# Optimization experiments

Measured on AMD Instinct MI355X. Metric: run time of the kernel, lower is better.

Reference implementation:

```python
import jax, jax.numpy as jnp
import numpy as np

B, N, F_IN = 8, 4096, 32
NRP = 1024
D_MODEL = 512
K = 64  # max_num_neighbors
STAGE_CFG = ((1024, 0.05), (256, 0.3), (64, 0.5))  # (num_samples=ceil(0.25*N_in), radius)


def fps(pos, m):
    """Farthest point sampling of m points from pos (N,3), deterministic start at 0."""
    d = jnp.sum((pos - pos[0]) ** 2, axis=-1)
    idxs = jnp.zeros((m,), jnp.int32)
    def body(i, carry):
        idxs, d = carry
        nxt = jnp.argmax(d).astype(jnp.int32)
        d = jnp.minimum(d, jnp.sum((pos - pos[nxt]) ** 2, axis=-1))
        return (idxs.at[i].set(nxt), d)
    idxs, _ = jax.lax.fori_loop(1, m, body, (idxs, d))
    return idxs


def apply_mlp(h, ws, bs):
    for w, b in zip(ws[:-1], bs[:-1]):
        h = jax.nn.relu(h @ w + b)
    return h @ ws[-1] + bs[-1]


def sa_stage(x, pos, m, r, ws, bs):
    """SAModule: FPS -> radius neighbors (<=K) -> PointNetConv (gather, MLP, max-scatter)."""
    idx = jax.vmap(lambda p: fps(p, m))(pos)                          # (B,m)
    pos_s = jnp.take_along_axis(pos, idx[..., None], axis=1)          # (B,m,3)
    d2 = jnp.sum((pos_s[:, :, None, :] - pos[:, None, :, :]) ** 2, -1)  # (B,m,N)
    neg = jnp.where(d2 <= r * r, -d2, -jnp.inf)
    vals, nbr = jax.lax.top_k(neg, K)                                 # (B,m,K) nearest within r
    valid = vals > -jnp.inf                                           # self always valid (d2=0)
    x_j = jax.vmap(lambda xb, nb: xb[nb])(x, nbr)                     # (B,m,K,F) gather
    p_j = jax.vmap(lambda pb, nb: pb[nb])(pos, nbr)                   # (B,m,K,3)
    h = jnp.concatenate([x_j, p_j - pos_s[:, :, None, :]], axis=-1)   # message input
    h = apply_mlp(h, ws, bs)
    h = jnp.where(valid[..., None], h, -jnp.inf)
    return jnp.max(h, axis=2), pos_s                                  # max aggregation


def _forward(point_cloud_features, point_cloud, emb_table, point_id_emb, stage_params):
    x = emb_table[point_cloud_features[..., 0]]                       # (B,N,F_IN)
    x = x.at[:, :NRP].add(point_id_emb)
    pos = point_cloud
    for (m, r), (ws, bs) in zip(STAGE_CFG, stage_params):
        x, pos = sa_stage(x, pos, m, r, ws, bs)
    return x, pos                                                     # (B,64,D_MODEL), (B,64,3)


def setup_inputs() -> dict:
    key = jax.random.key(0)
    ks = iter(jax.random.split(key, 64))
    def nrm(shape, s=0.05):
        return s * jax.random.normal(next(ks), shape, dtype=jnp.float32)
    inp = {
        "point_cloud_features": jax.random.randint(next(ks), (B, N, 1), 0, 3),
        "point_cloud": jax.random.uniform(next(ks), (B, N, 3), dtype=jnp.float32),
        "emb_table": nrm((3, F_IN), 1.0),
        "point_id_emb": nrm((1, NRP, F_IN), 1.0),
    }
    dims = {"s1": [3 + F_IN, 64, 64, 64], "s2": [64 + 3, 128, 128, 256], "s3": [256 + 3, 256, 512, D_MODEL]}
    for s, d in dims.items():
        for i in range(3):
            inp[f"{s}w{i}"] = nrm((d[i], d[i + 1]))
            inp[f"{s}b{i}"] = jnp.zeros((d[i + 1],), jnp.float32)
    return inp


def reference(point_cloud_features, point_cloud, emb_table, point_id_emb,
              s1w0, s1b0, s1w1, s1b1, s1w2, s1b2,
              s2w0, s2b0, s2w1, s2b1, s2w2, s2b2,
              s3w0, s3b0, s3w1, s3b1, s3w2, s3b2):
    stage_params = [
        ([s1w0, s1w1, s1w2], [s1b0, s1b1, s1b2]),
        ([s2w0, s2w1, s2w2], [s2b0, s2b1, s2b2]),
        ([s3w0, s3w1, s3w2], [s3b0, s3b1, s3b2]),
    ]
    return _forward(point_cloud_features, point_cloud, emb_table, point_id_emb, stage_params)
```

## Files before the change

kernel.cpp:

```cpp
#include <hip/hip_runtime.h>

#define DEVI static __device__ __forceinline__

constexpr int B = 8;
constexpr int N0 = 4096;
constexpr int KNB = 64;

typedef float f32x2 __attribute__((ext_vector_type(2)));

DEVI float dist2f(float ax, float ay, float az, float bx, float by, float bz) {
#pragma clang fp contract(off)
  float dx = ax - bx;
  float dy = ay - by;
  float dz = az - bz;
  return (dx * dx + dy * dy) + dz * dz;
}
DEVI f32x2 dist2v(f32x2 ax, f32x2 ay, f32x2 az, float bx, float by, float bz) {
#pragma clang fp contract(off)
  f32x2 dx = ax - bx;
  f32x2 dy = ay - by;
  f32x2 dz = az - bz;
  return (dx * dx + dy * dy) + dz * dz;
}

DEVI unsigned long long packMinKey(float v, int i) {
  return ((unsigned long long)__float_as_uint(v) << 32) | (unsigned int)i;
}

template <int CTRL, int RM>
DEVI float dppMaxF32(float v) {
  int o = __builtin_amdgcn_update_dpp(__float_as_int(v), __float_as_int(v),
                                      CTRL, RM, 0xf, false);
  return fmaxf(v, __int_as_float(o));
}
DEVI float waveMaxF32(float v) {
  v = dppMaxF32<0x111, 0xf>(v);
  v = dppMaxF32<0x112, 0xf>(v);
  v = dppMaxF32<0x114, 0xf>(v);
  v = dppMaxF32<0x118, 0xf>(v);
  v = dppMaxF32<0x142, 0xa>(v);
  v = dppMaxF32<0x143, 0xc>(v);
  return __int_as_float(__builtin_amdgcn_readlane(__float_as_int(v), 63));
}
template <int CTRL, int RM>
DEVI unsigned dppMinU32(unsigned v) {
  int o = __builtin_amdgcn_update_dpp((int)v, (int)v, CTRL, RM, 0xf, false);
  unsigned ov = (unsigned)o;
  return v < ov ? v : ov;
}
DEVI unsigned waveMinU32(unsigned v) {
  v = dppMinU32<0x111, 0xf>(v);
  v = dppMinU32<0x112, 0xf>(v);
  v = dppMinU32<0x114, 0xf>(v);
  v = dppMinU32<0x118, 0xf>(v);
  v = dppMinU32<0x142, 0xa>(v);
  v = dppMinU32<0x143, 0xc>(v);
  return (unsigned)__builtin_amdgcn_readlane((int)v, 63);
}


DEVI void x0_body(const int* __restrict__ feat, const float* __restrict__ emb,
                  const float* __restrict__ pid, float* __restrict__ x0buf,
                  int bx, int t) {
  int gid = bx * 256 + t;
  if (gid >= B * N0 * 32) return;
  int c = gid & 31;
  int bn = gid >> 5;
  int n = bn & (N0 - 1);
  int f = feat[bn];
  float v = emb[f * 32 + c];
  if (n < 1024) v += pid[n * 32 + c];
  x0buf[gid] = v;
}

template <int NPTS, int M, int BLK>
DEVI void fps_body(char* smem, const float* __restrict__ pos,
                   float* __restrict__ pos_out, int b, int t) {
  constexpr int EPT = NPTS / BLK;
  constexpr int EP2 = EPT / 2;
  constexpr int NW = BLK / 64;
  float4* posl = (float4*)smem;
  float4* outp = (float4*)(smem + (size_t)NPTS * 16);
  unsigned long long* redk =
      (unsigned long long*)(smem + (size_t)(NPTS + M) * 16);
  const float* pb = pos + (size_t)b * NPTS * 3;
  f32x2 px[EP2], py[EP2], pz[EP2], d[EP2];
#pragma unroll
  for (int e = 0; e < EP2; ++e) {
    int i0 = t + (2 * e) * BLK;
    int i1 = t + (2 * e + 1) * BLK;
    float x0 = pb[i0 * 3 + 0], y0 = pb[i0 * 3 + 1], z0 = pb[i0 * 3 + 2];
    float x1 = pb[i1 * 3 + 0], y1 = pb[i1 * 3 + 1], z1 = pb[i1 * 3 + 2];
    px[e] = (f32x2){x0, x1};
    py[e] = (f32x2){y0, y1};
    pz[e] = (f32x2){z0, z1};
    posl[i0] = make_float4(x0, y0, z0, 0.f);
    posl[i1] = make_float4(x1, y1, z1, 0.f);
  }
  float sx = pb[0], sy = pb[1], sz = pb[2];
  if (t == 0) outp[0] = make_float4(sx, sy, sz, 0.f);
  f32x2 m2 = (f32x2){-1.f, -1.f};
#pragma unroll
  for (int e = 0; e < EP2; ++e) {
    d[e] = dist2v(px[e], py[e], pz[e], sx, sy, sz);
    m2.x = fmaxf(m2.x, d[e].x);
    m2.y = fmaxf(m2.y, d[e].y);
  }
  for (int it = 1; it < M; ++it) {
    const float vstar = waveMaxF32(fmaxf(m2.x, m2.y));
    unsigned cand = 0xffffffffu;
#pragma unroll
    for (int e = 0; e < EP2; ++e) {
      unsigned c0 = (d[e].x == vstar) ? (unsigned)(t + (2 * e) * BLK) : 0xffffffffu;
      unsigned c1 = (d[e].y == vstar) ? (unsigned)(t + (2 * e + 1) * BLK) : 0xffffffffu;
      cand = cand < c0 ? cand : c0;
      cand = cand < c1 ? cand : c1;
    }
    cand = waveMinU32(cand);
    unsigned sel;
    if constexpr (NW > 1) {
      if ((t & 63) == 0) {
        unsigned long long key =
            ((unsigned long long)__float_as_uint(vstar) << 32) |
            (unsigned)(0x7fffffffu - cand);
        redk[(it & 1) * NW + (t >> 6)] = key;
      }
      __syncthreads();
      unsigned long long kk = redk[(it & 1) * NW + 0];
#pragma unroll
      for (int w = 1; w < NW; ++w) {
        unsigned long long o = redk[(it & 1) * NW + w];
        kk = (kk > o) ? kk : o;
      }
      sel = 0x7fffffffu - (unsigned)(kk & 0xffffffffULL);
    } else {
      sel = cand;
    }
    float4 sp = posl[sel];
    if (t == 0) outp[it] = sp;
    m2 = (f32x2){-1.f, -1.f};
#pragma unroll
    for (int e = 0; e < EP2; ++e) {
      f32x2 nd = dist2v(px[e], py[e], pz[e], sp.x, sp.y, sp.z);
      d[e].x = fminf(d[e].x, nd.x);
      d[e].y = fminf(d[e].y, nd.y);
      m2.x = fmaxf(m2.x, d[e].x);
      m2.y = fmaxf(m2.y, d[e].y);
    }
  }
  if constexpr (NW > 1) __syncthreads();
  for (int m = t; m < M; m += BLK) {
    float4 q = outp[m];
    pos_out[(size_t)(b * M + m) * 3 + 0] = q.x;
    pos_out[(size_t)(b * M + m) * 3 + 1] = q.y;
    pos_out[(size_t)(b * M + m) * 3 + 2] = q.z;
  }
}

template <int NPTS, int M>
DEVI void radius_body(char* smem, const float* __restrict__ pos,
                      const float* __restrict__ pos_s, float r2,
                      int* __restrict__ nbr, int* __restrict__ cnt, int blk,
                      int t) {
  unsigned long long* candkey = (unsigned long long*)smem;
  int* ctrp = (int*)(smem + (size_t)NPTS * 8);
  const int b = blk / M;
  const float* pb = pos + (size_t)b * NPTS * 3;
  const float cx = pos_s[(size_t)blk * 3 + 0];
  const float cy = pos_s[(size_t)blk * 3 + 1];
  const float cz = pos_s[(size_t)blk * 3 + 2];
  if (t == 0) *ctrp = 0;
  __syncthreads();
  for (int j = t; j < NPTS; j += 256) {
    float d2 = dist2f(pb[j * 3 + 0], pb[j * 3 + 1], pb[j * 3 + 2], cx, cy, cz);
    if (d2 <= r2) {
      int p = atomicAdd(ctrp, 1);
      candkey[p] = packMinKey(d2, j);
      if (p < KNB) nbr[(size_t)blk * KNB + p] = j;
    }
  }
  __syncthreads();
  const int c = *ctrp;
  if (c <= KNB) {
    if (t == 0) cnt[blk] = c;
    return;
  }
  for (int s = t; s < c; s += 256) {
    unsigned long long mykey = candkey[s];
    int rank = 0;
#pragma unroll 4
    for (int j = 0; j < c; ++j) {
      rank += (candkey[j] < mykey) ? 1 : 0;
    }
    if (rank < KNB)
      nbr[(size_t)blk * KNB + rank] = (int)(unsigned)(mykey & 0xffffffffULL);
  }
  if (t == 0) cnt[blk] = KNB;
}

DEVI void conv1_body(char* smem, const float* __restrict__ x0buf,
                     const float* __restrict__ pos,
                     const float* __restrict__ pos_s,
                     const int* __restrict__ nbr, const int* __restrict__ cntp,
                     const float* __restrict__ w0, const float* __restrict__ b0,
                     const float* __restrict__ w1, const float* __restrict__ b1,
                     const float* __restrict__ w2, const float* __restrict__ b2,
                     float* __restrict__ x1, int blk, int t) {
  float(*ins)[36] = (float(*)[36])smem;
  float(*hh)[65] = (float(*)[65])(smem + 576);
  float(*sred)[65] = (float(*)[65])(smem + 1616);
  const int slot = t >> 6;
  const int ch = t & 63;
  const int b = blk >> 10;
  const int c = cntp[blk];
  const float cx = pos_s[(size_t)blk * 3 + 0];
  const float cy = pos_s[(size_t)blk * 3 + 1];
  const float cz = pos_s[(size_t)blk * 3 + 2];
  float best = -__builtin_inff();
  for (int r0 = 0; r0 < c; r0 += 4) {
    const int r = r0 + slot;
    const bool act = r < c;
    const int j = nbr[(size_t)blk * KNB + (act ? r : 0)];
    if (ch < 32) {
      ins[slot][ch] = x0buf[((size_t)(b * N0) + j) * 32 + ch];
    } else if (ch < 35) {
      float pv = pos[((size_t)(b * N0) + j) * 3 + (ch - 32)];
      float cv = (ch == 32) ? cx : (ch == 33) ? cy : cz;
      ins[slot][ch] = pv - cv;
    }
    __syncthreads();
    float v = b0[ch];
#pragma unroll
    for (int i = 0; i < 35; ++i) v = fmaf(ins[slot][i], w0[i * 64 + ch], v);
    v = fmaxf(v, 0.f);
    hh[slot][ch] = v;
    __syncthreads();
    float v2 = b1[ch];
#pragma unroll
    for (int i = 0; i < 64; ++i) v2 = fmaf(hh[slot][i], w1[i * 64 + ch], v2);
    v2 = fmaxf(v2, 0.f);
    __syncthreads();
    hh[slot][ch] = v2;
    __syncthreads();
    float v3 = b2[ch];
#pragma unroll
    for (int i = 0; i < 64; ++i) v3 = fmaf(hh[slot][i], w2[i * 64 + ch], v3);
    if (act) best = fmaxf(best, v3);
    __syncthreads();
  }
  sred[slot][ch] = best;
  __syncthreads();
  if (t < 64) {
    float v = sred[0][t];
#pragma unroll
    for (int s = 1; s < 4; ++s) v = fmaxf(v, sred[s][t]);
    x1[(size_t)blk * 64 + t] = v;
  }
}

DEVI void conv2_body(char* smem, const float* __restrict__ x1,
                     const float* __restrict__ pos1,
                     const float* __restrict__ pos2,
                     const int* __restrict__ nbr, const int* __restrict__ cntp,
                     const float* __restrict__ w0, const float* __restrict__ b0,
                     const float* __restrict__ w1, const float* __restrict__ b1,
                     const float* __restrict__ w2, const float* __restrict__ b2,
                     float* __restrict__ x2, int blk, int t) {
  float(*msg)[68] = (float(*)[68])smem;
  float(*h)[128] = (float(*)[128])(smem + 17408);
  float(*red)[256] = (float(*)[256])(smem + 17408 + 32768);
  const int b = blk >> 8;
  const int c = cntp[blk];
  const float cx = pos2[(size_t)blk * 3 + 0];
  const float cy = pos2[(size_t)blk * 3 + 1];
  const float cz = pos2[(size_t)blk * 3 + 2];
  for (int idx = t; idx < 64 * 68; idx += 256) {
    int r = idx / 68;
    int k = idx - r * 68;
    float v = 0.f;
    if (r < c && k < 67) {
      int j = nbr[(size_t)blk * KNB + r];
      if (k < 64) {
        v = x1[((size_t)(b * 1024) + j) * 64 + k];
      } else {
        float pv = pos1[((size_t)(b * 1024) + j) * 3 + (k - 64)];
        v = pv - ((k == 64) ? cx : (k == 65) ? cy : cz);
      }
    }
    msg[r][k] = v;
  }
  __syncthreads();
  const int rg = t >> 5;
  const int cg = t & 31;
  {
    float acc[8][4] = {};
    for (int i4 = 0; i4 < 16; ++i4) {
      float wv[4][4];
#pragma unroll
      for (int k = 0; k < 4; ++k) {
        float4 q = *(const float4*)&w0[(size_t)(i4 * 4 + k) * 128 + cg * 4];
        wv[k][0] = q.x; wv[k][1] = q.y; wv[k][2] = q.z; wv[k][3] = q.w;
      }
#pragma unroll
      for (int rr = 0; rr < 8; ++rr) {
        float4 aq = *(const float4*)&msg[rg * 8 + rr][i4 * 4];
        float a[4] = {aq.x, aq.y, aq.z, aq.w};
#pragma unroll
        for (int k = 0; k < 4; ++k)
#pragma unroll
          for (int cc = 0; cc < 4; ++cc)
            acc[rr][cc] = fmaf(a[k], wv[k][cc], acc[rr][cc]);
      }
    }
#pragma unroll
    for (int i = 64; i < 67; ++i) {
      float wv[4];
#pragma unroll
      for (int cc = 0; cc < 4; ++cc) wv[cc] = w0[(size_t)i * 128 + cg * 4 + cc];
#pragma unroll
      for (int rr = 0; rr < 8; ++rr) {
        float a = msg[rg * 8 + rr][i];
#pragma unroll
        for (int cc = 0; cc < 4; ++cc) acc[rr][cc] = fmaf(a, wv[cc], acc[rr][cc]);
      }
    }
#pragma unroll
    for (int rr = 0; rr < 8; ++rr)
#pragma unroll
      for (int cc = 0; cc < 4; ++cc)
        h[rg * 8 + rr][cg * 4 + cc] = fmaxf(acc[rr][cc] + b0[cg * 4 + cc], 0.f);
  }
  __syncthreads();
  {
    float acc[8][4] = {};
    for (int i4 = 0; i4 < 32; ++i4) {
      float wv[4][4];
#pragma unroll
      for (int k = 0; k < 4; ++k) {
        float4 q = *(const float4*)&w1[(size_t)(i4 * 4 + k) * 128 + cg * 4];
        wv[k][0] = q.x; wv[k][1] = q.y; wv[k][2] = q.z; wv[k][3] = q.w;
      }
#pragma unroll
      for (int rr = 0; rr < 8; ++rr) {
        float4 aq = *(const float4*)&h[rg * 8 + rr][i4 * 4];
        float a[4] = {aq.x, aq.y, aq.z, aq.w};
#pragma unroll
        for (int k = 0; k < 4; ++k)
#pragma unroll
          for (int cc = 0; cc < 4; ++cc)
            acc[rr][cc] = fmaf(a[k], wv[k][cc], acc[rr][cc]);
      }
    }
    __syncthreads();
#pragma unroll
    for (int rr = 0; rr < 8; ++rr)
#pragma unroll
      for (int cc = 0; cc < 4; ++cc)
        h[rg * 8 + rr][cg * 4 + cc] = fmaxf(acc[rr][cc] + b1[cg * 4 + cc], 0.f);
  }
  __syncthreads();
  {
    float acc[8][8] = {};
    for (int i4 = 0; i4 < 32; ++i4) {
      float wv[4][8];
#pragma unroll
      for (int k = 0; k < 4; ++k) {
        float4 q0 = *(const float4*)&w2[(size_t)(i4 * 4 + k) * 256 + cg * 8];
        float4 q1 = *(const float4*)&w2[(size_t)(i4 * 4 + k) * 256 + cg * 8 + 4];
        wv[k][0] = q0.x; wv[k][1] = q0.y; wv[k][2] = q0.z; wv[k][3] = q0.w;
        wv[k][4] = q1.x; wv[k][5] = q1.y; wv[k][6] = q1.z; wv[k][7] = q1.w;
      }
#pragma unroll
      for (int rr = 0; rr < 8; ++rr) {
        float4 aq = *(const float4*)&h[rg * 8 + rr][i4 * 4];
        float a[4] = {aq.x, aq.y, aq.z, aq.w};
#pragma unroll
        for (int k = 0; k < 4; ++k)
#pragma unroll
          for (int cc = 0; cc < 8; ++cc)
            acc[rr][cc] = fmaf(a[k], wv[k][cc], acc[rr][cc]);
      }
    }
    float mx[8];
#pragma unroll
    for (int cc = 0; cc < 8; ++cc) mx[cc] = -__builtin_inff();
#pragma unroll
    for (int rr = 0; rr < 8; ++rr) {
      if (rg * 8 + rr < c) {
#pragma unroll
        for (int cc = 0; cc < 8; ++cc)
          mx[cc] = fmaxf(mx[cc], acc[rr][cc] + b2[cg * 8 + cc]);
      }
    }
#pragma unroll
    for (int cc = 0; cc < 8; ++cc) red[rg][cg * 8 + cc] = mx[cc];
  }
  __syncthreads();
  {
    float v = red[0][t];
#pragma unroll
    for (int g = 1; g < 8; ++g) v = fmaxf(v, red[g][t]);
    x2[(size_t)blk * 256 + t] = v;
  }
}


__global__ void __launch_bounds__(256) l1_kernel(
    const float* __restrict__ pos, float* __restrict__ pos1,
    const int* __restrict__ feat, const float* __restrict__ emb,
    const float* __restrict__ pid, float* __restrict__ x0buf) {
  __shared__ __attribute__((aligned(16))) char smem[81984];
  if (blockIdx.x < 8) {
    fps_body<4096, 1024, 256>(smem, pos, pos1, blockIdx.x, threadIdx.x);
  } else {
    x0_body(feat, emb, pid, x0buf, blockIdx.x - 8, threadIdx.x);
  }
}

__global__ void __launch_bounds__(256) l2_kernel(
    const float* __restrict__ pos1, float* __restrict__ pos2,
    const float* __restrict__ pos, float r2a, int* __restrict__ nbr1,
    int* __restrict__ cnt1) {
  __shared__ __attribute__((aligned(16))) char smem[33024];
  if (blockIdx.x < 8) {
    fps_body<1024, 256, 256>(smem, pos1, pos2, blockIdx.x, threadIdx.x);
  } else {
    radius_body<4096, 1024>(smem, pos, pos1, r2a, nbr1, cnt1, blockIdx.x - 8,
                            threadIdx.x);
  }
}

__global__ void __launch_bounds__(256) l3_kernel(
    const float* __restrict__ pos2, float* __restrict__ pos3, float r2b,
    int* __restrict__ nbr2, int* __restrict__ cnt2,
    const float* __restrict__ pos1, const float* __restrict__ x0buf,
    const float* __restrict__ pos, const int* __restrict__ nbr1,
    const int* __restrict__ cnt1, const float* __restrict__ w0,
    const float* __restrict__ b0, const float* __restrict__ w1,
    const float* __restrict__ b1, const float* __restrict__ w2,
    const float* __restrict__ b2, float* __restrict__ x1) {
  __shared__ __attribute__((aligned(16))) char smem[8448];
  if (blockIdx.x < 8) {
    if (threadIdx.x < 64)
      fps_body<256, 64, 64>(smem, pos2, pos3, blockIdx.x, threadIdx.x);
  } else if (blockIdx.x < 8 + 2048) {
    radius_body<1024, 256>(smem, pos1, pos2, r2b, nbr2, cnt2, blockIdx.x - 8,
                           threadIdx.x);
  } else {
    conv1_body(smem, x0buf, pos, pos1, nbr1, cnt1, w0, b0, w1, b1, w2, b2, x1,
               blockIdx.x - (8 + 2048), threadIdx.x);
  }
}

__global__ void __launch_bounds__(256) l4_kernel(
    const float* __restrict__ pos2, const float* __restrict__ pos3, float r2c,
    int* __restrict__ nbr3, int* __restrict__ cnt3,
    const float* __restrict__ x1, const float* __restrict__ pos1,
    const int* __restrict__ nbr2, const int* __restrict__ cnt2,
    const float* __restrict__ w0, const float* __restrict__ b0,
    const float* __restrict__ w1, const float* __restrict__ b1,
    const float* __restrict__ w2, const float* __restrict__ b2,
    float* __restrict__ x2) {
  __shared__ __attribute__((aligned(16))) char smem[58368];
  if (blockIdx.x < 512) {
    radius_body<256, 64>(smem, pos2, pos3, r2c, nbr3, cnt3, blockIdx.x,
                         threadIdx.x);
  } else {
    conv2_body(smem, x1, pos1, pos2, nbr2, cnt2, w0, b0, w1, b1, w2, b2, x2,
               blockIdx.x - 512, threadIdx.x);
  }
}

__global__ void __launch_bounds__(256) conv3_kernel(
    const float* __restrict__ x2, const float* __restrict__ pos2,
    const float* __restrict__ pos3, const int* __restrict__ nbr,
    const int* __restrict__ cntp,
    const float* __restrict__ w0, const float* __restrict__ b0,
    const float* __restrict__ w1, const float* __restrict__ b1,
    const float* __restrict__ w2, const float* __restrict__ b2,
    float* __restrict__ out) {
  __shared__ __attribute__((aligned(16))) float msg[16][260];
  __shared__ __attribute__((aligned(16))) float h[16][512];
  __shared__ float red[4][512];
  __shared__ float omax[512];
  const int blk = blockIdx.x;
  const int t = threadIdx.x;
  const int b = blk >> 6;
  const int c = cntp[blk];
  const float cx = pos3[(size_t)blk * 3 + 0];
  const float cy = pos3[(size_t)blk * 3 + 1];
  const float cz = pos3[(size_t)blk * 3 + 2];
  omax[t] = -__builtin_inff();
  omax[t + 256] = -__builtin_inff();
  const int rg = t >> 6;
  const int cg = t & 63;
  __syncthreads();
  for (int ch = 0; ch < 4; ++ch) {
    if (ch * 16 >= c) break;
    for (int idx = t; idx < 16 * 260; idx += 256) {
      int r = idx / 260;
      int k = idx - r * 260;
      int rglob = ch * 16 + r;
      float v = 0.f;
      if (rglob < c && k < 259) {
        int j = nbr[(size_t)blk * KNB + rglob];
        if (k < 256) {
          v = x2[((size_t)(b * 256) + j) * 256 + k];
        } else {
          float pv = pos2[((size_t)(b * 256) + j) * 3 + (k - 256)];
          v = pv - ((k == 256) ? cx : (k == 257) ? cy : cz);
        }
      }
      msg[r][k] = v;
    }
    __syncthreads();
    {
      float acc[4][4] = {};
      for (int i4 = 0; i4 < 64; ++i4) {
        float wv[4][4];
#pragma unroll
        for (int k = 0; k < 4; ++k) {
          float4 q = *(const float4*)&w0[(size_t)(i4 * 4 + k) * 256 + cg * 4];
          wv[k][0] = q.x; wv[k][1] = q.y; wv[k][2] = q.z; wv[k][3] = q.w;
        }
#pragma unroll
        for (int rr = 0; rr < 4; ++rr) {
          float4 aq = *(const float4*)&msg[rg * 4 + rr][i4 * 4];
          float a[4] = {aq.x, aq.y, aq.z, aq.w};
#pragma unroll
          for (int k = 0; k < 4; ++k)
#pragma unroll
            for (int cc = 0; cc < 4; ++cc)
              acc[rr][cc] = fmaf(a[k], wv[k][cc], acc[rr][cc]);
        }
      }
#pragma unroll
      for (int i = 256; i < 259; ++i) {
        float wv[4];
#pragma unroll
        for (int cc = 0; cc < 4; ++cc) wv[cc] = w0[(size_t)i * 256 + cg * 4 + cc];
#pragma unroll
        for (int rr = 0; rr < 4; ++rr) {
          float a = msg[rg * 4 + rr][i];
#pragma unroll
          for (int cc = 0; cc < 4; ++cc) acc[rr][cc] = fmaf(a, wv[cc], acc[rr][cc]);
        }
      }
#pragma unroll
      for (int rr = 0; rr < 4; ++rr)
#pragma unroll
        for (int cc = 0; cc < 4; ++cc)
          h[rg * 4 + rr][cg * 4 + cc] = fmaxf(acc[rr][cc] + b0[cg * 4 + cc], 0.f);
    }
    __syncthreads();
    {
      float acc[4][8] = {};
      for (int i4 = 0; i4 < 64; ++i4) {
        float wv[4][8];
#pragma unroll
        for (int k = 0; k < 4; ++k) {
          float4 q0 = *(const float4*)&w1[(size_t)(i4 * 4 + k) * 512 + cg * 8];
          float4 q1 = *(const float4*)&w1[(size_t)(i4 * 4 + k) * 512 + cg * 8 + 4];
          wv[k][0] = q0.x; wv[k][1] = q0.y; wv[k][2] = q0.z; wv[k][3] = q0.w;
          wv[k][4] = q1.x; wv[k][5] = q1.y; wv[k][6] = q1.z; wv[k][7] = q1.w;
        }
#pragma unroll
        for (int rr = 0; rr < 4; ++rr) {
          float4 aq = *(const float4*)&h[rg * 4 + rr][i4 * 4];
          float a[4] = {aq.x, aq.y, aq.z, aq.w};
#pragma unroll
          for (int k = 0; k < 4; ++k)
#pragma unroll
            for (int cc = 0; cc < 8; ++cc)
              acc[rr][cc] = fmaf(a[k], wv[k][cc], acc[rr][cc]);
        }
      }
      __syncthreads();
#pragma unroll
      for (int rr = 0; rr < 4; ++rr)
#pragma unroll
        for (int cc = 0; cc < 8; ++cc)
          h[rg * 4 + rr][cg * 8 + cc] = fmaxf(acc[rr][cc] + b1[cg * 8 + cc], 0.f);
    }
    __syncthreads();
    {
      float acc[4][8] = {};
      for (int i4 = 0; i4 < 128; ++i4) {
        float wv[4][8];
#pragma unroll
        for (int k = 0; k < 4; ++k) {
          float4 q0 = *(const float4*)&w2[(size_t)(i4 * 4 + k) * 512 + cg * 8];
          float4 q1 = *(const float4*)&w2[(size_t)(i4 * 4 + k) * 512 + cg * 8 + 4];
          wv[k][0] = q0.x; wv[k][1] = q0.y; wv[k][2] = q0.z; wv[k][3] = q0.w;
          wv[k][4] = q1.x; wv[k][5] = q1.y; wv[k][6] = q1.z; wv[k][7] = q1.w;
        }
#pragma unroll
        for (int rr = 0; rr < 4; ++rr) {
          float4 aq = *(const float4*)&h[rg * 4 + rr][i4 * 4];
          float a[4] = {aq.x, aq.y, aq.z, aq.w};
#pragma unroll
          for (int k = 0; k < 4; ++k)
#pragma unroll
            for (int cc = 0; cc < 8; ++cc)
              acc[rr][cc] = fmaf(a[k], wv[k][cc], acc[rr][cc]);
        }
      }
      float mx[8];
#pragma unroll
      for (int cc = 0; cc < 8; ++cc) mx[cc] = -__builtin_inff();
#pragma unroll
      for (int rr = 0; rr < 4; ++rr) {
        if (ch * 16 + rg * 4 + rr < c) {
#pragma unroll
          for (int cc = 0; cc < 8; ++cc)
            mx[cc] = fmaxf(mx[cc], acc[rr][cc] + b2[cg * 8 + cc]);
        }
      }
#pragma unroll
      for (int cc = 0; cc < 8; ++cc) red[rg][cg * 8 + cc] = mx[cc];
    }
    __syncthreads();
    for (int k = t; k < 512; k += 256) {
      float v = omax[k];
#pragma unroll
      for (int g = 0; g < 4; ++g) v = fmaxf(v, red[g][k]);
      omax[k] = v;
    }
    __syncthreads();
  }
  out[(size_t)blk * 512 + t] = omax[t];
  out[(size_t)blk * 512 + t + 256] = omax[t + 256];
}

extern "C" void kernel_launch(void* const* d_in, const int* in_sizes, int n_in,
                              void* d_out, int out_size, void* d_ws, size_t ws_size,
                              hipStream_t stream) {
  const int* feat = (const int*)d_in[0];
  const float* pos = (const float*)d_in[1];
  const float* emb = (const float*)d_in[2];
  const float* pid = (const float*)d_in[3];
  const float* s1w0 = (const float*)d_in[4];
  const float* s1b0 = (const float*)d_in[5];
  const float* s1w1 = (const float*)d_in[6];
  const float* s1b1 = (const float*)d_in[7];
  const float* s1w2 = (const float*)d_in[8];
  const float* s1b2 = (const float*)d_in[9];
  const float* s2w0 = (const float*)d_in[10];
  const float* s2b0 = (const float*)d_in[11];
  const float* s2w1 = (const float*)d_in[12];
  const float* s2b1 = (const float*)d_in[13];
  const float* s2w2 = (const float*)d_in[14];
  const float* s2b2 = (const float*)d_in[15];
  const float* s3w0 = (const float*)d_in[16];
  const float* s3b0 = (const float*)d_in[17];
  const float* s3w1 = (const float*)d_in[18];
  const float* s3b1 = (const float*)d_in[19];
  const float* s3w2 = (const float*)d_in[20];
  const float* s3b2 = (const float*)d_in[21];
  (void)in_sizes; (void)n_in; (void)out_size; (void)ws_size;

  char* ws = (char*)d_ws;
  size_t off = 0;
  auto alloc = [&](size_t nbytes) {
    void* p = ws + off;
    off = (off + nbytes + 255) & ~(size_t)255;
    return p;
  };
  float* x0 = (float*)alloc((size_t)B * N0 * 32 * 4);
  float* pos1 = (float*)alloc((size_t)B * 1024 * 3 * 4);
  int* nbr1 = (int*)alloc((size_t)B * 1024 * KNB * 4);
  int* cnt1 = (int*)alloc((size_t)B * 1024 * 4);
  float* x1 = (float*)alloc((size_t)B * 1024 * 64 * 4);
  float* pos2 = (float*)alloc((size_t)B * 256 * 3 * 4);
  int* nbr2 = (int*)alloc((size_t)B * 256 * KNB * 4);
  int* cnt2 = (int*)alloc((size_t)B * 256 * 4);
  float* x2 = (float*)alloc((size_t)B * 256 * 256 * 4);
  int* nbr3 = (int*)alloc((size_t)B * 64 * KNB * 4);
  int* cnt3 = (int*)alloc((size_t)B * 64 * 4);

  float* xout = (float*)d_out;
  float* pos3 = xout + (size_t)B * 64 * 512;

  const float r2a = (float)(0.05 * 0.05);
  const float r2b = (float)(0.3 * 0.3);
  const float r2c = (float)(0.5 * 0.5);

  l1_kernel<<<8 + 4096, 256, 0, stream>>>(pos, pos1, feat, emb, pid, x0);
  l2_kernel<<<8 + 8192, 256, 0, stream>>>(pos1, pos2, pos, r2a, nbr1, cnt1);
  l3_kernel<<<8 + 2048 + 8192, 256, 0, stream>>>(
      pos2, pos3, r2b, nbr2, cnt2, pos1, x0, pos, nbr1, cnt1,
      s1w0, s1b0, s1w1, s1b1, s1w2, s1b2, x1);
  l4_kernel<<<512 + 2048, 256, 0, stream>>>(
      pos2, pos3, r2c, nbr3, cnt3, x1, pos1, nbr2, cnt2,
      s2w0, s2b0, s2w1, s2b1, s2w2, s2b2, x2);
  conv3_kernel<<<B * 64, 256, 0, stream>>>(x2, pos2, pos3, nbr3, cnt3,
                                           s3w0, s3b0, s3w1, s3b1, s3w2, s3b2, xout);
}
```

Measured before the change: 1.517 ms.

## Run stage-3 PointNet MLP on bf16 MFMA with split hi/lo precision

Replaces the scalar-FMA conv3 kernel with one that uses 16x16x32 bf16 MFMA instructions. Each fp32 operand is split into bf16 hi and lo parts, and three MFMAs per tile keep accuracy close to fp32. Per-call pack kernels pre-swizzle the stage-3 weights into fragment layout. The kernel processes all 64 neighbors at once, tiles layer 2 and layer 3 by output chunk, and uses a cross-wave max reduction. It adds three small kernel launches and some precision risk from the bf16x3 emulation.

After: 1.460 ms. -3.7%, faster.

```diff
diff --git a/kernel.cpp b/kernel.cpp
--- a/kernel.cpp
+++ b/kernel.cpp
@@ -7,6 +7,8 @@
 constexpr int KNB = 64;
 
 typedef float f32x2 __attribute__((ext_vector_type(2)));
+typedef float f32x4 __attribute__((ext_vector_type(4)));
+typedef short bf16x8 __attribute__((ext_vector_type(8)));
 
 DEVI float dist2f(float ax, float ay, float az, float bx, float by, float bz) {
 #pragma clang fp contract(off)
@@ -56,6 +58,23 @@
   v = dppMinU32<0x142, 0xa>(v);
   v = dppMinU32<0x143, 0xc>(v);
   return (unsigned)__builtin_amdgcn_readlane((int)v, 63);
+}
+
+DEVI unsigned short bfhi(float x) {
+  unsigned u = __float_as_uint(x);
+  return (unsigned short)((u + 0x7FFFu + ((u >> 16) & 1u)) >> 16);
+}
+DEVI float bf2f(unsigned short h) { return __uint_as_float(((unsigned)h) << 16); }
+DEVI void mkfrag(const float* p, bf16x8& hi, bf16x8& lo) {
+#pragma unroll
+  for (int e = 0; e < 8; ++e) {
+    float x = p[e];
+    unsigned short h = bfhi(x);
+    float r = x - bf2f(h);
+    unsigned short l2 = bfhi(r);
+    hi[e] = (short)h;
+    lo[e] = (short)l2;
+  }
 }
 
 
@@ -471,165 +490,170 @@
   }
 }
 
-__global__ void __launch_bounds__(256) conv3_kernel(
+__global__ void __launch_bounds__(256) pack_kernel(
+    const float* __restrict__ W, int Kreal, int KS, int N,
+    unsigned short* __restrict__ hi, unsigned short* __restrict__ lo) {
+  int gid = blockIdx.x * 256 + threadIdx.x;
+  int total = (N / 16) * KS * 64 * 8;
+  if (gid >= total) return;
+  int e = gid & 7;
+  int l = (gid >> 3) & 63;
+  int rest = gid >> 9;
+  int ks = rest % KS;
+  int nt = rest / KS;
+  int n = nt * 16 + (l & 15);
+  int k = ks * 32 + (l >> 4) * 8 + e;
+  float val = (k < Kreal) ? W[(size_t)k * N + n] : 0.f;
+  unsigned short h = bfhi(val);
+  float r = val - bf2f(h);
+  hi[gid] = h;
+  lo[gid] = bfhi(r);
+}
+
+__global__ void __launch_bounds__(256) conv3_mfma(
     const float* __restrict__ x2, const float* __restrict__ pos2,
     const float* __restrict__ pos3, const int* __restrict__ nbr,
     const int* __restrict__ cntp,
-    const float* __restrict__ w0, const float* __restrict__ b0,
-    const float* __restrict__ w1, const float* __restrict__ b1,
-    const float* __restrict__ w2, const float* __restrict__ b2,
-    float* __restrict__ out) {
-  __shared__ __attribute__((aligned(16))) float msg[16][260];
-  __shared__ __attribute__((aligned(16))) float h[16][512];
-  __shared__ float red[4][512];
-  __shared__ float omax[512];
+    const unsigned short* __restrict__ w0h, const unsigned short* __restrict__ w0l,
+    const float* __restrict__ b0,
+    const unsigned short* __restrict__ w1h, const unsigned short* __restrict__ w1l,
+    const float* __restrict__ b1,
+    const unsigned short* __restrict__ w2h, const unsigned short* __restrict__ w2l,
+    const float* __restrict__ b2, float* __restrict__ out) {
+  __shared__ __attribute__((aligned(16))) float h1s[64 * 268];
+  __shared__ __attribute__((aligned(16))) float h2cs[64 * 140];
+  __shared__ __attribute__((aligned(16))) float msgcs[64 * 44];
   const int blk = blockIdx.x;
   const int t = threadIdx.x;
   const int b = blk >> 6;
   const int c = cntp[blk];
+  const int w = t >> 6;
+  const int lane = t & 63;
+  const int cb = lane & 15;
+  const int kb = lane >> 4;
   const float cx = pos3[(size_t)blk * 3 + 0];
   const float cy = pos3[(size_t)blk * 3 + 1];
   const float cz = pos3[(size_t)blk * 3 + 2];
-  omax[t] = -__builtin_inff();
-  omax[t + 256] = -__builtin_inff();
-  const int rg = t >> 6;
-  const int cg = t & 63;
-  __syncthreads();
+  const int mrow = w * 16 + cb;
+
+  f32x4 acc1[16];
+#pragma unroll
+  for (int nt = 0; nt < 16; ++nt) acc1[nt] = (f32x4){0.f, 0.f, 0.f, 0.f};
+  for (int ks = 0; ks < 9; ++ks) {
+#pragma unroll
+    for (int i = 0; i < 8; ++i) {
+      int idx = t + i * 256;
+      int row = idx >> 5;
+      int col = idx & 31;
+      int kg = ks * 32 + col;
+      int j = nbr[(size_t)blk * KNB + (row < c ? row : c - 1)];
+      float v = 0.f;
+      if (kg < 256) {
+        v = x2[((size_t)(b * 256) + j) * 256 + kg];
+      } else if (kg < 259) {
+        float pv = pos2[((size_t)(b * 256) + j) * 3 + (kg - 256)];
+        v = pv - ((kg == 256) ? cx : (kg == 257) ? cy : cz);
+      }
+      msgcs[row * 44 + col] = v;
+    }
+    __syncthreads();
+    bf16x8 ahi, alo;
+    mkfrag(&msgcs[mrow * 44 + kb * 8], ahi, alo);
+#pragma unroll
+    for (int nt = 0; nt < 16; ++nt) {
+      size_t off = ((size_t)(nt * 9 + ks) * 64 + lane) * 8;
+      bf16x8 bhi = *(const bf16x8*)(w0h + off);
+      bf16x8 blo = *(const bf16x8*)(w0l + off);
+      acc1[nt] = __builtin_amdgcn_mfma_f32_16x16x32_bf16(ahi, bhi, acc1[nt], 0, 0, 0);
+      acc1[nt] = __builtin_amdgcn_mfma_f32_16x16x32_bf16(alo, bhi, acc1[nt], 0, 0, 0);
+      acc1[nt] = __builtin_amdgcn_mfma_f32_16x16x32_bf16(ahi, blo, acc1[nt], 0, 0, 0);
+    }
+    __syncthreads();
+  }
+  {
+    const int mw = w * 16 + kb * 4;
+#pragma unroll
+    for (int nt = 0; nt < 16; ++nt) {
+      float bias = b0[nt * 16 + cb];
+#pragma unroll
+      for (int r = 0; r < 4; ++r)
+        h1s[(mw + r) * 268 + nt * 16 + cb] = fmaxf(acc1[nt][r] + bias, 0.f);
+    }
+  }
+  __syncthreads();
+
+  f32x4 acc3[32];
+#pragma unroll
+  for (int nt = 0; nt < 32; ++nt) acc3[nt] = (f32x4){0.f, 0.f, 0.f, 0.f};
   for (int ch = 0; ch < 4; ++ch) {
-    if (ch * 16 >= c) break;
-    for (int idx = t; idx < 16 * 260; idx += 256) {
-      int r = idx / 260;
-      int k = idx - r * 260;
-      int rglob = ch * 16 + r;
-      float v = 0.f;
-      if (rglob < c && k < 259) {
-        int j = nbr[(size_t)blk * KNB + rglob];
-        if (k < 256) {
-          v = x2[((size_t)(b * 256) + j) * 256 + k];
-        } else {
-          float pv = pos2[((size_t)(b * 256) + j) * 3 + (k - 256)];
-          v = pv - ((k == 256) ? cx : (k == 257) ? cy : cz);
-        }
-      }
-      msg[r][k] = v;
-    }
-    __syncthreads();
+    f32x4 acc2[8];
+#pragma unroll
+    for (int nt = 0; nt < 8; ++nt) acc2[nt] = (f32x4){0.f, 0.f, 0.f, 0.f};
+#pragma unroll
+    for (int ks = 0; ks < 8; ++ks) {
+      bf16x8 ahi, alo;
+      mkfrag(&h1s[mrow * 268 + ks * 32 + kb * 8], ahi, alo);
+#pragma unroll
+      for (int nt = 0; nt < 8; ++nt) {
+        size_t off = ((size_t)((ch * 8 + nt) * 8 + ks) * 64 + lane) * 8;
+        bf16x8 bhi = *(const bf16x8*)(w1h + off);
+        bf16x8 blo = *(const bf16x8*)(w1l + off);
+        acc2[nt] = __builtin_amdgcn_mfma_f32_16x16x32_bf16(ahi, bhi, acc2[nt], 0, 0, 0);
+        acc2[nt] = __builtin_amdgcn_mfma_f32_16x16x32_bf16(alo, bhi, acc2[nt], 0, 0, 0);
+        acc2[nt] = __builtin_amdgcn_mfma_f32_16x16x32_bf16(ahi, blo, acc2[nt], 0, 0, 0);
+      }
+    }
     {
-      float acc[4][4] = {};
-      for (int i4 = 0; i4 < 64; ++i4) {
-        float wv[4][4];
-#pragma unroll
-        for (int k = 0; k < 4; ++k) {
-          float4 q = *(const float4*)&w0[(size_t)(i4 * 4 + k) * 256 + cg * 4];
-          wv[k][0] = q.x; wv[k][1] = q.y; wv[k][2] = q.z; wv[k][3] = q.w;
-        }
-#pragma unroll
-        for (int rr = 0; rr < 4; ++rr) {
-          float4 aq = *(const float4*)&msg[rg * 4 + rr][i4 * 4];
-          float a[4] = {aq.x, aq.y, aq.z, aq.w};
-#pragma unroll
-          for (int k = 0; k < 4; ++k)
-#pragma unroll
-            for (int cc = 0; cc < 4; ++cc)
-              acc[rr][cc] = fmaf(a[k], wv[k][cc], acc[rr][cc]);
-        }
-      }
-#pragma unroll
-      for (int i = 256; i < 259; ++i) {
-        float wv[4];
-#pragma unroll
-        for (int cc = 0; cc < 4; ++cc) wv[cc] = w0[(size_t)i * 256 + cg * 4 + cc];
-#pragma unroll
-        for (int rr = 0; rr < 4; ++rr) {
-          float a = msg[rg * 4 + rr][i];
-#pragma unroll
-          for (int cc = 0; cc < 4; ++cc) acc[rr][cc] = fmaf(a, wv[cc], acc[rr][cc]);
-        }
-      }
-#pragma unroll
-      for (int rr = 0; rr < 4; ++rr)
-#pragma unroll
-        for (int cc = 0; cc < 4; ++cc)
-          h[rg * 4 + rr][cg * 4 + cc] = fmaxf(acc[rr][cc] + b0[cg * 4 + cc], 0.f);
-    }
-    __syncthreads();
-    {
-      float acc[4][8] = {};
-      for (int i4 = 0; i4 < 64; ++i4) {
-        float wv[4][8];
-#pragma unroll
-        for (int k = 0; k < 4; ++k) {
-          float4 q0 = *(const float4*)&w1[(size_t)(i4 * 4 + k) * 512 + cg * 8];
-          float4 q1 = *(const float4*)&w1[(size_t)(i4 * 4 + k) * 512 + cg * 8 + 4];
-          wv[k][0] = q0.x; wv[k][1] = q0.y; wv[k][2] = q0.z; wv[k][3] = q0.w;
-          wv[k][4] = q1.x; wv[k][5] = q1.y; wv[k][6] = q1.z; wv[k][7] = q1.w;
-        }
-#pragma unroll
-        for (int rr = 0; rr < 4; ++rr) {
-          float4 aq = *(const float4*)&h[rg * 4 + rr][i4 * 4];
-          float a[4] = {aq.x, aq.y, aq.z, aq.w};
-#pragma unroll
-          for (int k = 0; k < 4; ++k)
-#pragma unroll
-            for (int cc = 0; cc < 8; ++cc)
-              acc[rr][cc] = fmaf(a[k], wv[k][cc], acc[rr][cc]);
-        }
-      }
-      __syncthreads();
-#pragma unroll
-      for (int rr = 0; rr < 4; ++rr)
-#pragma unroll
-        for (int cc = 0; cc < 8; ++cc)
-          h[rg * 4 + rr][cg * 8 + cc] = fmaxf(acc[rr][cc] + b1[cg * 8 + cc], 0.f);
-    }
-    __syncthreads();
-    {
-      float acc[4][8] = {};
-      for (int i4 = 0; i4 < 128; ++i4) {
-        float wv[4][8];
-#pragma unroll
-        for (int k = 0; k < 4; ++k) {
-          float4 q0 = *(const float4*)&w2[(size_t)(i4 * 4 + k) * 512 + cg * 8];
-          float4 q1 = *(const float4*)&w2[(size_t)(i4 * 4 + k) * 512 + cg * 8 + 4];
-          wv[k][0] = q0.x; wv[k][1] = q0.y; wv[k][2] = q0.z; wv[k][3] = q0.w;
-          wv[k][4] = q1.x; wv[k][5] = q1.y; wv[k][6] = q1.z; wv[k][7] = q1.w;
-        }
-#pragma unroll
-        for (int rr = 0; rr < 4; ++rr) {
-          float4 aq = *(const float4*)&h[rg * 4 + rr][i4 * 4];
-          float a[4] = {aq.x, aq.y, aq.z, aq.w};
-#pragma unroll
-          for (int k = 0; k < 4; ++k)
-#pragma unroll
-            for (int cc = 0; cc < 8; ++cc)
-              acc[rr][cc] = fmaf(a[k], wv[k][cc], acc[rr][cc]);
-        }
-      }
-      float mx[8];
-#pragma unroll
-      for (int cc = 0; cc < 8; ++cc) mx[cc] = -__builtin_inff();
-#pragma unroll
-      for (int rr = 0; rr < 4; ++rr) {
-        if (ch * 16 + rg * 4 + rr < c) {
-#pragma unroll
-          for (int cc = 0; cc < 8; ++cc)
-            mx[cc] = fmaxf(mx[cc], acc[rr][cc] + b2[cg * 8 + cc]);
-        }
-      }
-#pragma unroll
-      for (int cc = 0; cc < 8; ++cc) red[rg][cg * 8 + cc] = mx[cc];
-    }
-    __syncthreads();
-    for (int k = t; k < 512; k += 256) {
-      float v = omax[k];
-#pragma unroll
-      for (int g = 0; g < 4; ++g) v = fmaxf(v, red[g][k]);
-      omax[k] = v;
-    }
-    __syncthreads();
-  }
-  out[(size_t)blk * 512 + t] = omax[t];
-  out[(size_t)blk * 512 + t + 256] = omax[t + 256];
+      const int mw = w * 16 + kb * 4;
+#pragma unroll
+      for (int nt = 0; nt < 8; ++nt) {
+        float bias = b1[ch * 128 + nt * 16 + cb];
+#pragma unroll
+        for (int r = 0; r < 4; ++r)
+          h2cs[(mw + r) * 140 + nt * 16 + cb] = fmaxf(acc2[nt][r] + bias, 0.f);
+      }
+    }
+    __syncthreads();
+#pragma unroll
+    for (int ks3 = 0; ks3 < 4; ++ks3) {
+      bf16x8 ahi, alo;
+      mkfrag(&h2cs[mrow * 140 + ks3 * 32 + kb * 8], ahi, alo);
+#pragma unroll
+      for (int nt = 0; nt < 32; ++nt) {
+        size_t off = ((size_t)(nt * 16 + ch * 4 + ks3) * 64 + lane) * 8;
+        bf16x8 bhi = *(const bf16x8*)(w2h + off);
+        bf16x8 blo = *(const bf16x8*)(w2l + off);
+        acc3[nt] = __builtin_amdgcn_mfma_f32_16x16x32_bf16(ahi, bhi, acc3[nt], 0, 0, 0);
+        acc3[nt] = __builtin_amdgcn_mfma_f32_16x16x32_bf16(alo, bhi, acc3[nt], 0, 0, 0);
+        acc3[nt] = __builtin_amdgcn_mfma_f32_16x16x32_bf16(ahi, blo, acc3[nt], 0, 0, 0);
+      }
+    }
+    __syncthreads();
+  }
+
+  float* redw = h1s;
+  {
+    const int mw = w * 16 + kb * 4;
+#pragma unroll
+    for (int nt = 0; nt < 32; ++nt) {
+      float bias = b2[nt * 16 + cb];
+      float mx = -__builtin_inff();
+#pragma unroll
+      for (int r = 0; r < 4; ++r) {
+        if (mw + r < c) mx = fmaxf(mx, acc3[nt][r] + bias);
+      }
+      redw[(w * 4 + kb) * 512 + nt * 16 + cb] = mx;
+    }
+  }
+  __syncthreads();
+#pragma unroll
+  for (int half = 0; half < 2; ++half) {
+    int col = t + half * 256;
+    float v = redw[col];
+#pragma unroll
+    for (int g = 1; g < 16; ++g) v = fmaxf(v, redw[g * 512 + col]);
+    out[(size_t)blk * 512 + col] = v;
+  }
 }
 
 extern "C" void kernel_launch(void* const* d_in, const int* in_sizes, int n_in,
@@ -677,6 +701,15 @@
   float* x2 = (float*)alloc((size_t)B * 256 * 256 * 4);
   int* nbr3 = (int*)alloc((size_t)B * 64 * KNB * 4);
   int* cnt3 = (int*)alloc((size_t)B * 64 * 4);
+  const int T0 = 16 * 9 * 64 * 8;
+  const int T1 = 32 * 8 * 64 * 8;
+  const int T2 = 32 * 16 * 64 * 8;
+  unsigned short* w0h = (unsigned short*)alloc((size_t)T0 * 2);
+  unsigned short* w0l = (unsigned short*)alloc((size_t)T0 * 2);
+  unsigned short* w1h = (unsigned short*)alloc((size_t)T1 * 2);
+  unsigned short* w1l = (unsigned short*)alloc((size_t)T1 * 2);
+  unsigned short* w2h = (unsigned short*)alloc((size_t)T2 * 2);
+  unsigned short* w2l = (unsigned short*)alloc((size_t)T2 * 2);
 
   float* xout = (float*)d_out;
   float* pos3 = xout + (size_t)B * 64 * 512;
@@ -684,6 +717,10 @@
   const float r2a = (float)(0.05 * 0.05);
   const float r2b = (float)(0.3 * 0.3);
   const float r2c = (float)(0.5 * 0.5);
+
+  pack_kernel<<<(T0 + 255) / 256, 256, 0, stream>>>(s3w0, 259, 9, 256, w0h, w0l);
+  pack_kernel<<<(T1 + 255) / 256, 256, 0, stream>>>(s3w1, 256, 8, 512, w1h, w1l);
+  pack_kernel<<<(T2 + 255) / 256, 256, 0, stream>>>(s3w2, 512, 16, 512, w2h, w2l);
 
   l1_kernel<<<8 + 4096, 256, 0, stream>>>(pos, pos1, feat, emb, pid, x0);
   l2_kernel<<<8 + 8192, 256, 0, stream>>>(pos1, pos2, pos, r2a, nbr1, cnt1);
@@ -693,6 +730,7 @@
   l4_kernel<<<512 + 2048, 256, 0, stream>>>(
       pos2, pos3, r2c, nbr3, cnt3, x1, pos1, nbr2, cnt2,
       s2w0, s2b0, s2w1, s2b1, s2w2, s2b2, x2);
-  conv3_kernel<<<B * 64, 256, 0, stream>>>(x2, pos2, pos3, nbr3, cnt3,
-                                           s3w0, s3b0, s3w1, s3b1, s3w2, s3b2, xout);
-}
+  conv3_mfma<<<B * 64, 256, 0, stream>>>(x2, pos2, pos3, nbr3, cnt3,
+                                         w0h, w0l, s3b0, w1h, w1l, s3b1,
+                                         w2h, w2l, s3b2, xout);
+}
```
